# Performance work log

Hardware: AMD Instinct MI355X
Metric: run time of the kernel (lower is better)

## Reference

```python
import jax, jax.numpy as jnp
import numpy as np

B, N, FIN, E, OUT, NH = 8, 1024, 128, 128, 128, 8
HD = E // NH  # head_dim = 16


def setup_inputs() -> dict:
    key = jax.random.key(0)
    ks = jax.random.split(key, 8)
    s = 0.05
    H = jax.random.normal(ks[0], (B, N, FIN), jnp.float32)
    # binary adjacency (sparse-ish graph), stored dense float as the module expects
    A = (jax.random.uniform(ks[1], (B, N, N)) < 0.05).astype(jnp.float32)
    W_lin = jax.random.normal(ks[2], (FIN, E), jnp.float32) * s
    b_lin = jnp.zeros((E,), jnp.float32)
    # nn.MultiheadAttention packed in-projection (q,k,v) and out-projection
    W_in = jax.random.normal(ks[3], (E, 3 * E), jnp.float32) * s
    b_in = jnp.zeros((3 * E,), jnp.float32)
    W_out = jax.random.normal(ks[4], (E, E), jnp.float32) * s
    b_out = jnp.zeros((E,), jnp.float32)
    W_fin = jax.random.normal(ks[5], (E, OUT), jnp.float32) * s
    b_fin = jnp.zeros((OUT,), jnp.float32)
    return dict(H=H, A=A, W_lin=W_lin, b_lin=b_lin, W_in=W_in, b_in=b_in,
                W_out=W_out, b_out=b_out, W_fin=W_fin, b_fin=b_fin)


def reference(H, A, W_lin, b_lin, W_in, b_in, W_out, b_out, W_fin, b_fin):
    # input projection: Linear(128, embed_dim)
    Hp = H @ W_lin + b_lin                                   # (B,N,E)
    # adjacency-gated attention weights: bmm -> LeakyReLU(0.2) -> *A -> softmax
    s = jnp.einsum('bnd,bmd->bnm', Hp, Hp)                   # (B,N,N)
    s = jnp.where(s >= 0, s, 0.2 * s)
    attn_w = jax.nn.softmax(s * A, axis=-1)                  # (B,N,N)
    # nn.MultiheadAttention self-attention with float attn_mask (ADDED to scores)
    qkv = Hp @ W_in + b_in                                   # (B,N,3E)
    q, k, v = jnp.split(qkv, 3, axis=-1)
    q = q.reshape(B, N, NH, HD)
    k = k.reshape(B, N, NH, HD)
    v = v.reshape(B, N, NH, HD)
    scores = jnp.einsum('bnhd,bmhd->bhnm', q, k) / np.sqrt(HD).astype(np.float32)
    scores = scores + attn_w[:, None]                        # mask broadcast over heads
    p = jax.nn.softmax(scores, axis=-1)                      # (B,NH,N,N)
    o = jnp.einsum('bhnm,bmhd->bnhd', p, v).reshape(B, N, E)
    o = o @ W_out + b_out                                    # MHA out_proj
    # output linear; dropout is identity in eval mode
    return o @ W_fin + b_fin                                 # (B,N,OUT)
```

## Files before the change

### kernel.cpp

```cpp
#include <hip/hip_runtime.h>
#include <hip/hip_bf16.h>


using u16 = unsigned short;
typedef short bf16x8 __attribute__((ext_vector_type(8)));
typedef float f32x4 __attribute__((ext_vector_type(4)));
typedef _Float16 f16;
typedef _Float16 f16x4 __attribute__((ext_vector_type(4)));

#define MFMA16(a, b, c) __builtin_amdgcn_mfma_f32_16x16x16f16(a, b, c, 0, 0, 0)
#define MFMAB(a, b, c) __builtin_amdgcn_mfma_f32_16x16x32_bf16(a, b, c, 0, 0, 0)

__device__ __forceinline__ u16 f2b(float f) {
    unsigned u = __float_as_uint(f);
    return (u16)((u + 0x7fffu + ((u >> 16) & 1u)) >> 16);
}
__device__ __forceinline__ float b2f(u16 u) {
    return __uint_as_float(((unsigned)u) << 16);
}

__global__ void prep_hp(const float* __restrict__ H, const float* __restrict__ Wlin,
                        const float* __restrict__ Win,
                        const float* __restrict__ Wout, const float* __restrict__ Wfin,
                        const float* __restrict__ bout, const float* __restrict__ bfin,
                        const float* __restrict__ blin,
                        u16* __restrict__ WinTb, u16* __restrict__ WcombTb,
                        float* __restrict__ bcomb, float* __restrict__ rowsum,
                        u16* __restrict__ Hpb) {
    if (blockIdx.x < 64) {
        const int m0 = blockIdx.x * 128;
        const int t = threadIdx.x;
        const int wave = t >> 6, lane = t & 63;
        const int wm = (wave >> 1) * 64, wn = (wave & 1) * 64;
        const int m16 = lane & 15, kq = lane >> 4;
        f32x4 acc[4][4] = {};

#pragma unroll
        for (int kc = 0; kc < 4; ++kc) {
            bf16x8 af[4], bf[4];
#pragma unroll
            for (int i = 0; i < 4; ++i) {
                const float* ap = &H[(long long)(m0 + wm + i * 16 + m16) * 128 + kc * 32 + kq * 8];
                float4 u0 = *(const float4*)ap;
                float4 u1 = *(const float4*)(ap + 4);
                bf16x8 a;
                a[0] = (short)f2b(u0.x); a[1] = (short)f2b(u0.y);
                a[2] = (short)f2b(u0.z); a[3] = (short)f2b(u0.w);
                a[4] = (short)f2b(u1.x); a[5] = (short)f2b(u1.y);
                a[6] = (short)f2b(u1.z); a[7] = (short)f2b(u1.w);
                af[i] = a;
            }
#pragma unroll
            for (int j = 0; j < 4; ++j) {
                const int col = wn + j * 16 + m16;
                const int k0 = kc * 32 + kq * 8;
                bf16x8 bb;
#pragma unroll
                for (int e = 0; e < 8; ++e)
                    bb[e] = (short)f2b(Wlin[(long long)(k0 + e) * 128 + col]);
                bf[j] = bb;
            }
#pragma unroll
            for (int i = 0; i < 4; ++i)
#pragma unroll
                for (int j = 0; j < 4; ++j)
                    acc[i][j] = MFMAB(af[i], bf[j], acc[i][j]);
        }
#pragma unroll
        for (int i = 0; i < 4; ++i) {
#pragma unroll
            for (int r = 0; r < 4; ++r) {
                long long row = m0 + wm + i * 16 + kq * 4 + r;
#pragma unroll
                for (int j = 0; j < 4; ++j) {
                    int col = wn + j * 16 + m16;
                    Hpb[row * 128 + col] = f2b(acc[i][j][r] + blin[col]);
                }
            }
        }
        return;
    }
    int i = (blockIdx.x - 64) * 256 + threadIdx.x;
    if (i < 8192) rowsum[i] = 0.f;
    if (i >= 16384 && i < 65536) {
        int k = i - 16384;
        int r = k / 384, c = k - r * 384;
        WinTb[c * 128 + r] = f2b(Win[k]);
    } else if (i >= 65536) {
        int k = i - 65536;
        int o = k & 127, e = k >> 7;
        float s = 0.f;
        for (int kk = 0; kk < 128; ++kk)
            s = fmaf(Wout[e * 128 + kk], Wfin[kk * 128 + o], s);
        WcombTb[o * 128 + e] = f2b(s);
        if (e == 0) {
            float sb = bfin[o];
            for (int kk = 0; kk < 128; ++kk)
                sb = fmaf(bout[kk], Wfin[kk * 128 + o], sb);
            bcomb[o] = sb;
        }
    }
}

__global__ __launch_bounds__(256)
void mfma_qkvz(const u16* __restrict__ Hpb, const u16* __restrict__ WinTb,
               const float* __restrict__ bin, f16* __restrict__ Cq,
               const float* __restrict__ Aadj, u16* __restrict__ EZ,
               float* __restrict__ rowsum) {
    const int blk = blockIdx.x;
    const int t = threadIdx.x;
    const int wave = t >> 6, lane = t & 63;
    const int wm = (wave >> 1) * 64, wn = (wave & 1) * 64;
    const int m16 = lane & 15, kq = lane >> 4;
    f32x4 acc[4][4] = {};

    if (blk < 512) {
        const int b = blk >> 6, mt = (blk >> 3) & 7, nt = blk & 7;
        const u16* Ab = Hpb + (long long)b * 1024 * 128;
        const int m0 = mt * 128, n0 = nt * 128;
#pragma unroll
        for (int kc = 0; kc < 4; ++kc) {
            bf16x8 af[4], bf[4];
#pragma unroll
            for (int i = 0; i < 4; ++i)
                af[i] = *(const bf16x8*)&Ab[(long long)(m0 + wm + i * 16 + m16) * 128 + kc * 32 + kq * 8];
#pragma unroll
            for (int j = 0; j < 4; ++j)
                bf[j] = *(const bf16x8*)&Ab[(long long)(n0 + wn + j * 16 + m16) * 128 + kc * 32 + kq * 8];
#pragma unroll
            for (int i = 0; i < 4; ++i)
#pragma unroll
                for (int j = 0; j < 4; ++j)
                    acc[i][j] = MFMAB(af[i], bf[j], acc[i][j]);
        }
        const long long zb = (long long)b * 1024 * 1024;
#pragma unroll
        for (int i = 0; i < 4; ++i) {
#pragma unroll
            for (int r = 0; r < 4; ++r) {
                int row = m0 + wm + i * 16 + kq * 4 + r;
                float es = 0.f;
#pragma unroll
                for (int j = 0; j < 4; ++j) {
                    int col = n0 + wn + j * 16 + m16;
                    float v = acc[i][j][r];
                    v = v >= 0.f ? v : 0.2f * v;
                    if (Aadj[zb + (long long)row * 1024 + col] == 0.f) v = 0.f;
                    float ev = __expf(v);
                    EZ[zb + (long long)row * 1024 + col] = f2b(ev);
                    es += ev;
                }
#pragma unroll
                for (int off = 1; off < 16; off <<= 1) es += __shfl_xor(es, off);
                if (m16 == 0) atomicAdd(&rowsum[b * 1024 + row], es);
            }
        }
    } else {
        const int q = blk - 512;
        const int mt = q & 63, slab = q >> 6;
        const int m0 = mt * 128;
        const u16* Bslab = WinTb + (long long)slab * 128 * 128;
#pragma unroll
        for (int kc = 0; kc < 4; ++kc) {
            bf16x8 af[4], bf[4];
#pragma unroll
            for (int i = 0; i < 4; ++i)
                af[i] = *(const bf16x8*)&Hpb[(long long)(m0 + wm + i * 16 + m16) * 128 + kc * 32 + kq * 8];
#pragma unroll
            for (int j = 0; j < 4; ++j)
                bf[j] = *(const bf16x8*)&Bslab[(long long)(wn + j * 16 + m16) * 128 + kc * 32 + kq * 8];
#pragma unroll
            for (int i = 0; i < 4; ++i)
#pragma unroll
                for (int j = 0; j < 4; ++j)
                    acc[i][j] = MFMAB(af[i], bf[j], acc[i][j]);
        }
        const float qscale = (slab == 0) ? 0.25f : 1.f;
#pragma unroll
        for (int i = 0; i < 4; ++i) {
#pragma unroll
            for (int r = 0; r < 4; ++r) {
                long long row = m0 + wm + i * 16 + kq * 4 + r;
#pragma unroll
                for (int j = 0; j < 4; ++j) {
                    int col = wn + j * 16 + m16;
                    float v = (acc[i][j][r] + bin[slab * 128 + col]) * qscale;
                    Cq[row * 384 + slab * 128 + col] = (f16)v;
                }
            }
        }
    }
}

__global__ __launch_bounds__(256)
void flash_mfma(const f16* __restrict__ qkv, const u16* __restrict__ ez,
                const float* __restrict__ rowsum, u16* __restrict__ ob) {
    const int bid = blockIdx.x;
    const int xcd = bid & 7;
    const int rr_ = bid >> 3;
    const int hpair = rr_ & 3;
    const int g = rr_ >> 2;
    const int pair = g * 8 + xcd;
    const int n0 = (pair & 15) * 64;
    const int b = pair >> 4;
    const int h0 = hpair * 2;
    const int t = threadIdx.x;
    const int w = t >> 6, lane = t & 63;
    const int qr16 = lane & 15, quad = lane >> 4;

    __shared__ u16 Ks[64 * 40];
    __shared__ u16 VTs[32 * 76];
    __shared__ u16 AWs[64 * 72];

    const int qrow_l = w * 16 + qr16;
    const long long qrow_g = b * 1024 + n0 + qrow_l;
    const float inv0 = 1.f / rowsum[qrow_g];

    f16x4 qf[2];
#pragma unroll
    for (int hh = 0; hh < 2; ++hh)
        qf[hh] = *(const f16x4*)&qkv[qrow_g * 384 + (h0 + hh) * 16 + quad * 4];

    f32x4 accO[2] = {};
    float lacc[2] = {0.f, 0.f};

    for (int st = 0; st < 16; ++st) {
        const int kb = st * 64;
        __syncthreads();
        {
            const int key = t >> 2, c8 = t & 3;
            *(uint4*)&Ks[key * 40 + c8 * 8] =
                *(const uint4*)&qkv[((long long)(b * 1024 + kb + key)) * 384 + 128 + h0 * 16 + c8 * 8];
            const f16* vsrc = &qkv[((long long)(b * 1024 + kb + key)) * 384 + 256 + h0 * 16 + c8 * 8];
            f16x4 v0 = *(const f16x4*)vsrc;
            f16x4 v1 = *(const f16x4*)(vsrc + 4);
            const int d0 = c8 * 8;
#pragma unroll
            for (int i = 0; i < 4; ++i) {
                VTs[(d0 + i) * 76 + key] = ((const u16*)&v0)[i];
                VTs[(d0 + 4 + i) * 76 + key] = ((const u16*)&v1)[i];
            }
        }
#pragma unroll
        for (int rr = 0; rr < 2; ++rr) {
            int idx = rr * 256 + t;
            int row = idx >> 3, c16 = idx & 7;
            *(uint4*)&AWs[row * 72 + c16 * 8] =
                *(const uint4*)&ez[((long long)(b * 1024 + n0 + row)) * 1024 + kb + c16 * 8];
        }
        __syncthreads();

#pragma unroll 2
        for (int kt = 0; kt < 4; ++kt) {
            ushort4 ue = *(const ushort4*)&AWs[qrow_l * 72 + kt * 16 + quad * 4];
            f32x4 aw0;
            aw0[0] = b2f(ue.x) * inv0; aw0[1] = b2f(ue.y) * inv0;
            aw0[2] = b2f(ue.z) * inv0; aw0[3] = b2f(ue.w) * inv0;
#pragma unroll
            for (int hh = 0; hh < 2; ++hh) {
                f16x4 kf = *(const f16x4*)&Ks[(kt * 16 + qr16) * 40 + hh * 16 + quad * 4];
                f32x4 s4 = MFMA16(kf, qf[hh], aw0);
                float p0 = __expf(s4[0]), p1 = __expf(s4[1]);
                float p2 = __expf(s4[2]), p3 = __expf(s4[3]);
                lacc[hh] += (p0 + p1) + (p2 + p3);
                f16x4 pf;
                pf[0] = (f16)p0; pf[1] = (f16)p1; pf[2] = (f16)p2; pf[3] = (f16)p3;
                f16x4 vf = *(const f16x4*)&VTs[(hh * 16 + qr16) * 76 + kt * 16 + quad * 4];
                accO[hh] = MFMA16(vf, pf, accO[hh]);
            }
        }
    }
#pragma unroll
    for (int hh = 0; hh < 2; ++hh) {
        float l = lacc[hh];
        l += __shfl_xor(l, 16);
        l += __shfl_xor(l, 32);
        float inv = 1.f / l;
        ushort4 st4;
        st4.x = f2b(accO[hh][0] * inv);
        st4.y = f2b(accO[hh][1] * inv);
        st4.z = f2b(accO[hh][2] * inv);
        st4.w = f2b(accO[hh][3] * inv);
        *(ushort4*)&ob[qrow_g * 128 + (h0 + hh) * 16 + quad * 4] = st4;
    }
}

__global__ __launch_bounds__(256)
void mfma_out(const u16* __restrict__ A, const u16* __restrict__ Bb,
              const float* __restrict__ bias, float* __restrict__ C) {
    const int m0 = blockIdx.x * 128;
    const int t = threadIdx.x;
    const int wave = t >> 6, lane = t & 63;
    const int wm = (wave >> 1) * 64, wn = (wave & 1) * 64;
    const int m16 = lane & 15, kq = lane >> 4;
    f32x4 acc[4][4] = {};

#pragma unroll
    for (int kc = 0; kc < 4; ++kc) {
        bf16x8 af[4], bf[4];
#pragma unroll
        for (int i = 0; i < 4; ++i)
            af[i] = *(const bf16x8*)&A[(long long)(m0 + wm + i * 16 + m16) * 128 + kc * 32 + kq * 8];
#pragma unroll
        for (int j = 0; j < 4; ++j)
            bf[j] = *(const bf16x8*)&Bb[(long long)(wn + j * 16 + m16) * 128 + kc * 32 + kq * 8];
#pragma unroll
        for (int i = 0; i < 4; ++i)
#pragma unroll
            for (int j = 0; j < 4; ++j)
                acc[i][j] = MFMAB(af[i], bf[j], acc[i][j]);
    }
#pragma unroll
    for (int i = 0; i < 4; ++i) {
#pragma unroll
        for (int r = 0; r < 4; ++r) {
            long long row = m0 + wm + i * 16 + kq * 4 + r;
#pragma unroll
            for (int j = 0; j < 4; ++j) {
                int col = wn + j * 16 + m16;
                C[row * 128 + col] = acc[i][j][r] + bias[col];
            }
        }
    }
}

extern "C" void kernel_launch(void* const* d_in, const int* in_sizes, int n_in,
                              void* d_out, int out_size, void* d_ws, size_t ws_size,
                              hipStream_t stream) {
    (void)in_sizes; (void)n_in; (void)out_size; (void)ws_size;
    const float* H    = (const float*)d_in[0];
    const float* Aadj = (const float*)d_in[1];
    const float* Wlin = (const float*)d_in[2];
    const float* blin = (const float*)d_in[3];
    const float* Win  = (const float*)d_in[4];
    const float* bin  = (const float*)d_in[5];
    const float* Wout = (const float*)d_in[6];
    const float* bout = (const float*)d_in[7];
    const float* Wfin = (const float*)d_in[8];
    const float* bfin = (const float*)d_in[9];
    float* out = (float*)d_out;
    char* ws = (char*)d_ws;

    u16*   WinTb   = (u16*)(ws + 0);
    u16*   WcombTb = (u16*)(ws + 98304);
    float* bcomb   = (float*)(ws + 131072);
    float* rowsum  = (float*)(ws + 131584);
    u16*   Hpb     = (u16*)(ws + 262144);
    f16*   qkv     = (f16*)(ws + 2359296);
    u16*   ob      = (u16*)(ws + 8650752);
    u16*   ez      = (u16*)(ws + 12845056);

    prep_hp<<<384, 256, 0, stream>>>(H, Wlin, Win, Wout, Wfin, bout, bfin,
                                     blin, WinTb, WcombTb, bcomb, rowsum, Hpb);
    mfma_qkvz<<<704, 256, 0, stream>>>(Hpb, WinTb, bin, qkv, Aadj, ez, rowsum);
    flash_mfma<<<512, 256, 0, stream>>>(qkv, ez, rowsum, ob);
    mfma_out<<<64, 256, 0, stream>>>(ob, WcombTb, bcomb, out);
}
```

Measured before the change: 157.6 us.

## Fuse output GEMM into flash kernel via atomic ticket tail blocks

Removes the separate output-projection kernel launch. The last 64 blocks of the attention kernel to finish, chosen by an atomic ticket counter, spin until all 512 blocks are done and then each computes one 128-row tile of the output GEMM. The score-tile block mapping in the qkvz kernel is also remapped to interleave batches across consecutive blocks. This saves a launch and its gap, but adds a grid-wide spin-wait that leaves the tail blocks idle, and it relies on all blocks being co-resident or scheduled in ticket order.

```diff
diff --git a/kernel.cpp b/kernel.cpp
--- a/kernel.cpp
+++ b/kernel.cpp
@@ -26,7 +26,7 @@
                         const float* __restrict__ blin,
                         u16* __restrict__ WinTb, u16* __restrict__ WcombTb,
                         float* __restrict__ bcomb, float* __restrict__ rowsum,
-                        u16* __restrict__ Hpb) {
+                        u16* __restrict__ Hpb, unsigned* __restrict__ ticket) {
     if (blockIdx.x < 64) {
         const int m0 = blockIdx.x * 128;
         const int t = threadIdx.x;
@@ -82,6 +82,7 @@
     }
     int i = (blockIdx.x - 64) * 256 + threadIdx.x;
     if (i < 8192) rowsum[i] = 0.f;
+    if (i == 8192) *ticket = 0;
     if (i >= 16384 && i < 65536) {
         int k = i - 16384;
         int r = k / 384, c = k - r * 384;
@@ -115,7 +116,8 @@
     f32x4 acc[4][4] = {};
 
     if (blk < 512) {
-        const int b = blk >> 6, mt = (blk >> 3) & 7, nt = blk & 7;
+        const int b = blk & 7, tile = blk >> 3;
+        const int mt = tile >> 3, nt = tile & 7;
         const u16* Ab = Hpb + (long long)b * 1024 * 128;
         const int m0 = mt * 128, n0 = nt * 128;
 #pragma unroll
@@ -194,7 +196,9 @@
 
 __global__ __launch_bounds__(256)
 void flash_mfma(const f16* __restrict__ qkv, const u16* __restrict__ ez,
-                const float* __restrict__ rowsum, u16* __restrict__ ob) {
+                const float* __restrict__ rowsum, u16* __restrict__ ob,
+                const u16* __restrict__ WcombTb, const float* __restrict__ bcomb,
+                float* __restrict__ out, unsigned* __restrict__ ticket) {
     const int bid = blockIdx.x;
     const int xcd = bid & 7;
     const int rr_ = bid >> 3;
@@ -211,6 +215,7 @@
     __shared__ u16 Ks[64 * 40];
     __shared__ u16 VTs[32 * 76];
     __shared__ u16 AWs[64 * 72];
+    __shared__ unsigned tk_s;
 
     const int qrow_l = w * 16 + qr16;
     const long long qrow_g = b * 1024 + n0 + qrow_l;
@@ -283,42 +288,54 @@
         st4.w = f2b(accO[hh][3] * inv);
         *(ushort4*)&ob[qrow_g * 128 + (h0 + hh) * 16 + quad * 4] = st4;
     }
-}
-
-__global__ __launch_bounds__(256)
-void mfma_out(const u16* __restrict__ A, const u16* __restrict__ Bb,
-              const float* __restrict__ bias, float* __restrict__ C) {
-    const int m0 = blockIdx.x * 128;
-    const int t = threadIdx.x;
-    const int wave = t >> 6, lane = t & 63;
-    const int wm = (wave >> 1) * 64, wn = (wave & 1) * 64;
-    const int m16 = lane & 15, kq = lane >> 4;
-    f32x4 acc[4][4] = {};
-
-#pragma unroll
-    for (int kc = 0; kc < 4; ++kc) {
-        bf16x8 af[4], bf[4];
-#pragma unroll
-        for (int i = 0; i < 4; ++i)
-            af[i] = *(const bf16x8*)&A[(long long)(m0 + wm + i * 16 + m16) * 128 + kc * 32 + kq * 8];
-#pragma unroll
-        for (int j = 0; j < 4; ++j)
-            bf[j] = *(const bf16x8*)&Bb[(long long)(wn + j * 16 + m16) * 128 + kc * 32 + kq * 8];
-#pragma unroll
-        for (int i = 0; i < 4; ++i)
+
+    __syncthreads();
+    if (t == 0) {
+        __threadfence();
+        tk_s = __hip_atomic_fetch_add(ticket, 1u, __ATOMIC_RELAXED,
+                                      __HIP_MEMORY_SCOPE_AGENT);
+    }
+    __syncthreads();
+    const unsigned tk = tk_s;
+    if (tk < 448u) return;
+    if (t == 0) {
+        while (__hip_atomic_load(ticket, __ATOMIC_RELAXED,
+                                 __HIP_MEMORY_SCOPE_AGENT) < 512u)
+            __builtin_amdgcn_s_sleep(8);
+        __threadfence();
+    }
+    __syncthreads();
+    {
+        const int m0 = (int)(tk - 448u) * 128;
+        const int wave = t >> 6;
+        const int wm = (wave >> 1) * 64, wn = (wave & 1) * 64;
+        const int m16 = lane & 15, kq = lane >> 4;
+        f32x4 acc[4][4] = {};
+#pragma unroll
+        for (int kc = 0; kc < 4; ++kc) {
+            bf16x8 af[4], bf[4];
+#pragma unroll
+            for (int i = 0; i < 4; ++i)
+                af[i] = *(const bf16x8*)&ob[(long long)(m0 + wm + i * 16 + m16) * 128 + kc * 32 + kq * 8];
 #pragma unroll
             for (int j = 0; j < 4; ++j)
-                acc[i][j] = MFMAB(af[i], bf[j], acc[i][j]);
-    }
-#pragma unroll
-    for (int i = 0; i < 4; ++i) {
-#pragma unroll
-        for (int r = 0; r < 4; ++r) {
-            long long row = m0 + wm + i * 16 + kq * 4 + r;
-#pragma unroll
-            for (int j = 0; j < 4; ++j) {
-                int col = wn + j * 16 + m16;
-                C[row * 128 + col] = acc[i][j][r] + bias[col];
+                bf[j] = *(const bf16x8*)&WcombTb[(long long)(wn + j * 16 + m16) * 128 + kc * 32 + kq * 8];
+#pragma unroll
+            for (int i = 0; i < 4; ++i)
+#pragma unroll
+                for (int j = 0; j < 4; ++j)
+                    acc[i][j] = MFMAB(af[i], bf[j], acc[i][j]);
+        }
+#pragma unroll
+        for (int i = 0; i < 4; ++i) {
+#pragma unroll
+            for (int r = 0; r < 4; ++r) {
+                long long row = m0 + wm + i * 16 + kq * 4 + r;
+#pragma unroll
+                for (int j = 0; j < 4; ++j) {
+                    int col = wn + j * 16 + m16;
+                    out[row * 128 + col] = acc[i][j][r] + bcomb[col];
+                }
             }
         }
     }
@@ -349,10 +366,12 @@
     f16*   qkv     = (f16*)(ws + 2359296);
     u16*   ob      = (u16*)(ws + 8650752);
     u16*   ez      = (u16*)(ws + 12845056);
+    unsigned* ticket = (unsigned*)(ws + 29622272);
 
     prep_hp<<<384, 256, 0, stream>>>(H, Wlin, Win, Wout, Wfin, bout, bfin,
-                                     blin, WinTb, WcombTb, bcomb, rowsum, Hpb);
+                                     blin, WinTb, WcombTb, bcomb, rowsum, Hpb,
+                                     ticket);
     mfma_qkvz<<<704, 256, 0, stream>>>(Hpb, WinTb, bin, qkv, Aadj, ez, rowsum);
-    flash_mfma<<<512, 256, 0, stream>>>(qkv, ez, rowsum, ob);
-    mfma_out<<<64, 256, 0, stream>>>(ob, WcombTb, bcomb, out);
-}
+    flash_mfma<<<512, 256, 0, stream>>>(qkv, ez, rowsum, ob, WcombTb, bcomb,
+                                        out, ticket);
+}
```

Result: slower. 178.8 us (+13.5%).
